# Performance work log

Measured on AMD Instinct MI355X. Metric: run time of the kernel, lower is better.

## Reference

```python
import jax, jax.numpy as jnp
import numpy as np

IN_FEATURES = 512
OUT_FEATURES = 128
KERNEL_DIM = 32
BATCH = 128


def setup_inputs() -> dict:
    key = jax.random.key(0)
    kx, kT = jax.random.split(key)
    x = jax.random.normal(kx, (BATCH, IN_FEATURES), dtype=jnp.float32)
    # nn.Parameter initialized with normal(0, 1)
    T = jax.random.normal(kT, (IN_FEATURES, OUT_FEATURES, KERNEL_DIM), dtype=jnp.float32)
    return {"x": x, "T": T}


def reference(x, T):
    B = x.shape[0]
    in_f, out_f, k_dim = T.shape
    # projection: [B, in] @ [in, out*k] -> [B, out, k]
    m = (x @ T.reshape(in_f, out_f * k_dim)).reshape(B, out_f, k_dim)
    # pairwise L1 distance over kernel dim: [B, B, out]
    # original: M = m[None], M_T = m[:, None]; norm = |M - M_T|.sum(3); o_b = exp(-norm).sum(0) - 1
    norm = jnp.abs(m[None, :, :, :] - m[:, None, :, :]).sum(axis=-1)  # [i=B, j=B, out]
    o_b = jnp.exp(-norm).sum(axis=0) - 1.0  # [B, out] (subtract self-distance term exp(0)=1)
    return jnp.concatenate([x, o_b], axis=1)  # [B, in + out]
```

## Files before the change

### kernel.cpp

```cpp
#include <hip/hip_runtime.h>

#define IN_F    512
#define NC      4096
#define OUT_COLS 640
#define B_SZ    128
#define KD      32
#define MO_PITCH 36

typedef __attribute__((ext_vector_type(8))) short  bf16x8;
typedef __attribute__((ext_vector_type(4))) float  f32x4;

static __device__ __forceinline__ unsigned short f2bfu(float f) {
    return (unsigned short)(__float_as_uint(f) >> 16);
}
static __device__ __forceinline__ unsigned int pack2(float lo, float hi) {
    return (__float_as_uint(lo) >> 16) | (__float_as_uint(hi) & 0xFFFF0000u);
}

__global__ __launch_bounds__(256) void prep_kernel(
    const float* __restrict__ x, float* __restrict__ out,
    unsigned short* __restrict__ xa)
{
    const int g = blockIdx.x * 256 + threadIdx.x;
    {
        int b = g >> 7, c4 = g & 127;
        float4 v = ((const float4*)x)[g];
        *(float4*)(out + b * OUT_COLS + c4 * 4) = v;
    }
    const int s = g >> 1, half = g & 1;
    const int mt = s >> 10, kt = (s >> 6) & 15, lane = s & 63;
    const int col = lane & 15, q = lane >> 4;
    float4 v = *(const float4*)(x + (mt * 16 + col) * IN_F + kt * 32 + q * 8 + half * 4);
    uint2 pv; pv.x = pack2(v.x, v.y); pv.y = pack2(v.z, v.w);
    *(uint2*)(xa + (size_t)s * 8 + half * 4) = pv;
}

__global__ __launch_bounds__(1024, 4) void fused_kernel(
    const unsigned short* __restrict__ xa,
    const float* __restrict__ T,
    float* __restrict__ out)
{
    __shared__ unsigned short bs[2 * 16 * 64 * 8];
    __shared__ float mo[B_SZ * MO_PITCH];
    __shared__ float psum[2 * 32 * 33];

    const int tid   = threadIdx.x;
    const int lane  = tid & 63;
    const int w     = tid >> 6;
    const int col   = lane & 15;
    const int q     = lane >> 4;
    const int o     = blockIdx.x >> 1;
    const int jhalf = blockIdx.x & 1;
    const int mt    = w >> 1, nt = w & 1;

    #pragma unroll
    for (int p = 0; p < 4; ++p) {
        int u  = tid + p * 1024;
        int kk = u >> 3, cq = u & 7;
        float4 v = *(const float4*)(T + (size_t)kk * NC + o * 32 + cq * 4);
        int kt = kk >> 5, qq = (kk >> 3) & 3, j = kk & 7;
        float e[4] = {v.x, v.y, v.z, v.w};
        #pragma unroll
        for (int r = 0; r < 4; ++r) {
            int nn = cq * 4 + r;
            int ln = qq * 16 + (nn & 15);
            bs[((((nn >> 4) * 16 + kt) * 64) + ln) * 8 + j] = f2bfu(e[r]);
        }
    }
    __syncthreads();

    f32x4 acc = {0.f, 0.f, 0.f, 0.f};
    const unsigned short* pa = xa + ((size_t)(mt * 16) * 64 + lane) * 8;
    const unsigned short* pb = bs + ((size_t)(nt * 16) * 64 + lane) * 8;
    #pragma unroll 4
    for (int kt = 0; kt < 16; ++kt) {
        bf16x8 af  = *(const bf16x8*)(pa + (size_t)kt * 512);
        bf16x8 bfr = *(const bf16x8*)(pb + (size_t)kt * 512);
        acc = __builtin_amdgcn_mfma_f32_16x16x32_bf16(af, bfr, acc, 0, 0, 0);
    }
    {
        float* dst = mo + (size_t)(mt * 16 + q * 4) * MO_PITCH + nt * 16 + col;
        dst[0 * MO_PITCH] = acc[0]; dst[1 * MO_PITCH] = acc[1];
        dst[2 * MO_PITCH] = acc[2]; dst[3 * MO_PITCH] = acc[3];
    }
    __syncthreads();

    const int jj5 = tid & 31;
    const int isl = tid >> 5;
    const int j0  = jhalf * 64 + jj5;

    float mj0[KD], mj1[KD];
    #pragma unroll
    for (int k4 = 0; k4 < 8; ++k4) {
        float4 a = *(const float4*)(mo + (size_t)j0 * MO_PITCH + k4 * 4);
        float4 b = *(const float4*)(mo + (size_t)(j0 + 32) * MO_PITCH + k4 * 4);
        mj0[k4*4+0] = a.x; mj0[k4*4+1] = a.y; mj0[k4*4+2] = a.z; mj0[k4*4+3] = a.w;
        mj1[k4*4+0] = b.x; mj1[k4*4+1] = b.y; mj1[k4*4+2] = b.z; mj1[k4*4+3] = b.w;
    }

    float s0 = 0.f, s1 = 0.f;
    #pragma unroll
    for (int ii = 0; ii < 4; ++ii) {
        const int i = isl * 4 + ii;
        float n0 = 0.f, n1 = 0.f;
        #pragma unroll
        for (int k4 = 0; k4 < 8; ++k4) {
            float4 v = *(const float4*)(mo + (size_t)i * MO_PITCH + k4 * 4);
            n0 += fabsf(mj0[k4*4+0] - v.x) + fabsf(mj0[k4*4+1] - v.y)
                + fabsf(mj0[k4*4+2] - v.z) + fabsf(mj0[k4*4+3] - v.w);
            n1 += fabsf(mj1[k4*4+0] - v.x) + fabsf(mj1[k4*4+1] - v.y)
                + fabsf(mj1[k4*4+2] - v.z) + fabsf(mj1[k4*4+3] - v.w);
        }
        s0 += __expf(-n0);
        s1 += __expf(-n1);
    }
    psum[jj5 * 33 + isl]        = s0;
    psum[1056 + jj5 * 33 + isl] = s1;
    __syncthreads();
    if (tid < 64) {
        int jsel = tid >> 5, jj = tid & 31;
        float tot = 0.f;
        #pragma unroll
        for (int u = 0; u < 32; ++u) tot += psum[jsel * 1056 + jj * 33 + u];
        out[(jhalf * 64 + jsel * 32 + jj) * OUT_COLS + IN_F + o] = tot - 1.0f;
    }
}

extern "C" void kernel_launch(void* const* d_in, const int* in_sizes, int n_in,
                              void* d_out, int out_size, void* d_ws, size_t ws_size,
                              hipStream_t stream) {
    const float* x = (const float*)d_in[0];
    const float* T = (const float*)d_in[1];
    float* out = (float*)d_out;
    unsigned short* xa = (unsigned short*)d_ws;

    prep_kernel<<<64, 256, 0, stream>>>(x, out, xa);
    fused_kernel<<<256, 1024, 0, stream>>>(xa, T, out);
}
```

Before: 71.06 us.

## Fuse prep into main kernel, halve block size, use fp16 packed L1 distances

Removes the separate prep kernel: the x copy into the output and the bf16 conversion of x now happen inside the fused kernel, with each block reading x from global memory and packing fragments in registers. Blocks shrink to 512 threads, so each wave computes two MFMA column tiles. The projection result is stored in shared memory as fp16, and the pairwise L1 distances use packed half2 subtract, abs and add instead of fp32. This saves a launch and halves the distance arithmetic, but fp16 accumulation of distances loses precision, and every block now re-reads and re-converts x.

```diff
diff --git a/kernel.cpp b/kernel.cpp
--- a/kernel.cpp
+++ b/kernel.cpp
@@ -1,14 +1,18 @@
 #include <hip/hip_runtime.h>
+#include <hip/hip_fp16.h>
 
 #define IN_F    512
 #define NC      4096
 #define OUT_COLS 640
 #define B_SZ    128
 #define KD      32
-#define MO_PITCH 36
+#define MOH_PITCH 72
 
 typedef __attribute__((ext_vector_type(8))) short  bf16x8;
 typedef __attribute__((ext_vector_type(4))) float  f32x4;
+
+union FragAB { unsigned int u[4]; bf16x8 s; };
+union H2x4   { uint4 u4; __half2 h[4]; };
 
 static __device__ __forceinline__ unsigned short f2bfu(float f) {
     return (unsigned short)(__float_as_uint(f) >> 16);
@@ -16,46 +20,38 @@
 static __device__ __forceinline__ unsigned int pack2(float lo, float hi) {
     return (__float_as_uint(lo) >> 16) | (__float_as_uint(hi) & 0xFFFF0000u);
 }
-
-__global__ __launch_bounds__(256) void prep_kernel(
-    const float* __restrict__ x, float* __restrict__ out,
-    unsigned short* __restrict__ xa)
-{
-    const int g = blockIdx.x * 256 + threadIdx.x;
-    {
-        int b = g >> 7, c4 = g & 127;
-        float4 v = ((const float4*)x)[g];
-        *(float4*)(out + b * OUT_COLS + c4 * 4) = v;
-    }
-    const int s = g >> 1, half = g & 1;
-    const int mt = s >> 10, kt = (s >> 6) & 15, lane = s & 63;
-    const int col = lane & 15, q = lane >> 4;
-    float4 v = *(const float4*)(x + (mt * 16 + col) * IN_F + kt * 32 + q * 8 + half * 4);
-    uint2 pv; pv.x = pack2(v.x, v.y); pv.y = pack2(v.z, v.w);
-    *(uint2*)(xa + (size_t)s * 8 + half * 4) = pv;
+static __device__ __forceinline__ __half2 habs2_(__half2 v) {
+    unsigned int u = *(unsigned int*)&v & 0x7FFF7FFFu;
+    return *(__half2*)&u;
 }
 
-__global__ __launch_bounds__(1024, 4) void fused_kernel(
-    const unsigned short* __restrict__ xa,
+__global__ __launch_bounds__(512, 2) void fused_kernel(
+    const float* __restrict__ x,
     const float* __restrict__ T,
     float* __restrict__ out)
 {
     __shared__ unsigned short bs[2 * 16 * 64 * 8];
-    __shared__ float mo[B_SZ * MO_PITCH];
-    __shared__ float psum[2 * 32 * 33];
+    __shared__ __half moh[B_SZ * MOH_PITCH];
+    __shared__ float psum[2 * 32 * 17];
 
     const int tid   = threadIdx.x;
     const int lane  = tid & 63;
-    const int w     = tid >> 6;
+    const int mt    = tid >> 6;
     const int col   = lane & 15;
     const int q     = lane >> 4;
     const int o     = blockIdx.x >> 1;
     const int jhalf = blockIdx.x & 1;
-    const int mt    = w >> 1, nt = w & 1;
+
+    if (tid < 64) {
+        int idx = blockIdx.x * 64 + tid;
+        int b = idx >> 7, c4 = idx & 127;
+        float4 v = ((const float4*)x)[idx];
+        *(float4*)(out + b * OUT_COLS + c4 * 4) = v;
+    }
 
     #pragma unroll
-    for (int p = 0; p < 4; ++p) {
-        int u  = tid + p * 1024;
+    for (int p = 0; p < 8; ++p) {
+        int u  = tid + p * 512;
         int kk = u >> 3, cq = u & 7;
         float4 v = *(const float4*)(T + (size_t)kk * NC + o * 32 + cq * 4);
         int kt = kk >> 5, qq = (kk >> 3) & 3, j = kk & 7;
@@ -63,65 +59,76 @@
         #pragma unroll
         for (int r = 0; r < 4; ++r) {
             int nn = cq * 4 + r;
-            int ln = qq * 16 + (nn & 15);
-            bs[((((nn >> 4) * 16 + kt) * 64) + ln) * 8 + j] = f2bfu(e[r]);
+            int slot = (((nn >> 4) * 16 + kt) * 64) + qq * 16 + (nn & 15);
+            bs[slot * 8 + j] = f2bfu(e[r]);
         }
     }
     __syncthreads();
 
-    f32x4 acc = {0.f, 0.f, 0.f, 0.f};
-    const unsigned short* pa = xa + ((size_t)(mt * 16) * 64 + lane) * 8;
-    const unsigned short* pb = bs + ((size_t)(nt * 16) * 64 + lane) * 8;
-    #pragma unroll 4
+    f32x4 acc0 = {0.f, 0.f, 0.f, 0.f}, acc1 = {0.f, 0.f, 0.f, 0.f};
+    const float* xrow = x + (size_t)(mt * 16 + col) * IN_F + q * 8;
+    #pragma unroll 8
     for (int kt = 0; kt < 16; ++kt) {
-        bf16x8 af  = *(const bf16x8*)(pa + (size_t)kt * 512);
-        bf16x8 bfr = *(const bf16x8*)(pb + (size_t)kt * 512);
-        acc = __builtin_amdgcn_mfma_f32_16x16x32_bf16(af, bfr, acc, 0, 0, 0);
+        float4 a0 = *(const float4*)(xrow + kt * 32);
+        float4 a1 = *(const float4*)(xrow + kt * 32 + 4);
+        FragAB af;
+        af.u[0] = pack2(a0.x, a0.y); af.u[1] = pack2(a0.z, a0.w);
+        af.u[2] = pack2(a1.x, a1.y); af.u[3] = pack2(a1.z, a1.w);
+        bf16x8 b0 = *(const bf16x8*)&bs[((kt      ) * 64 + lane) * 8];
+        bf16x8 b1 = *(const bf16x8*)&bs[((16 + kt) * 64 + lane) * 8];
+        acc0 = __builtin_amdgcn_mfma_f32_16x16x32_bf16(af.s, b0, acc0, 0, 0, 0);
+        acc1 = __builtin_amdgcn_mfma_f32_16x16x32_bf16(af.s, b1, acc1, 0, 0, 0);
     }
     {
-        float* dst = mo + (size_t)(mt * 16 + q * 4) * MO_PITCH + nt * 16 + col;
-        dst[0 * MO_PITCH] = acc[0]; dst[1 * MO_PITCH] = acc[1];
-        dst[2 * MO_PITCH] = acc[2]; dst[3 * MO_PITCH] = acc[3];
+        const int rowb = mt * 16 + q * 4;
+        #pragma unroll
+        for (int r = 0; r < 4; ++r) {
+            moh[(rowb + r) * MOH_PITCH + col]      = __float2half(acc0[r]);
+            moh[(rowb + r) * MOH_PITCH + 16 + col] = __float2half(acc1[r]);
+        }
     }
     __syncthreads();
 
     const int jj5 = tid & 31;
-    const int isl = tid >> 5;
+    const int isl = tid >> 4 >> 1;
     const int j0  = jhalf * 64 + jj5;
 
-    float mj0[KD], mj1[KD];
+    __half2 mj0[16], mj1[16];
     #pragma unroll
-    for (int k4 = 0; k4 < 8; ++k4) {
-        float4 a = *(const float4*)(mo + (size_t)j0 * MO_PITCH + k4 * 4);
-        float4 b = *(const float4*)(mo + (size_t)(j0 + 32) * MO_PITCH + k4 * 4);
-        mj0[k4*4+0] = a.x; mj0[k4*4+1] = a.y; mj0[k4*4+2] = a.z; mj0[k4*4+3] = a.w;
-        mj1[k4*4+0] = b.x; mj1[k4*4+1] = b.y; mj1[k4*4+2] = b.z; mj1[k4*4+3] = b.w;
+    for (int k16 = 0; k16 < 4; ++k16) {
+        H2x4 a, b;
+        a.u4 = *(const uint4*)&moh[j0 * MOH_PITCH + k16 * 8];
+        b.u4 = *(const uint4*)&moh[(j0 + 32) * MOH_PITCH + k16 * 8];
+        #pragma unroll
+        for (int h = 0; h < 4; ++h) { mj0[k16*4+h] = a.h[h]; mj1[k16*4+h] = b.h[h]; }
     }
 
     float s0 = 0.f, s1 = 0.f;
     #pragma unroll
-    for (int ii = 0; ii < 4; ++ii) {
-        const int i = isl * 4 + ii;
-        float n0 = 0.f, n1 = 0.f;
+    for (int ii = 0; ii < 8; ++ii) {
+        const int i = isl * 8 + ii;
+        __half2 n0 = __float2half2_rn(0.f), n1 = __float2half2_rn(0.f);
         #pragma unroll
-        for (int k4 = 0; k4 < 8; ++k4) {
-            float4 v = *(const float4*)(mo + (size_t)i * MO_PITCH + k4 * 4);
-            n0 += fabsf(mj0[k4*4+0] - v.x) + fabsf(mj0[k4*4+1] - v.y)
-                + fabsf(mj0[k4*4+2] - v.z) + fabsf(mj0[k4*4+3] - v.w);
-            n1 += fabsf(mj1[k4*4+0] - v.x) + fabsf(mj1[k4*4+1] - v.y)
-                + fabsf(mj1[k4*4+2] - v.z) + fabsf(mj1[k4*4+3] - v.w);
+        for (int k16 = 0; k16 < 4; ++k16) {
+            H2x4 mi; mi.u4 = *(const uint4*)&moh[i * MOH_PITCH + k16 * 8];
+            #pragma unroll
+            for (int h = 0; h < 4; ++h) {
+                n0 = __hadd2(n0, habs2_(__hsub2(mj0[k16*4+h], mi.h[h])));
+                n1 = __hadd2(n1, habs2_(__hsub2(mj1[k16*4+h], mi.h[h])));
+            }
         }
-        s0 += __expf(-n0);
-        s1 += __expf(-n1);
+        float2 f0 = __half22float2(n0), f1 = __half22float2(n1);
+        s0 += __expf(-(f0.x + f0.y));
+        s1 += __expf(-(f1.x + f1.y));
     }
-    psum[jj5 * 33 + isl]        = s0;
-    psum[1056 + jj5 * 33 + isl] = s1;
+    psum[jj5 * 17 + isl]       = s0;
+    psum[544 + jj5 * 17 + isl] = s1;
     __syncthreads();
     if (tid < 64) {
         int jsel = tid >> 5, jj = tid & 31;
         float tot = 0.f;
         #pragma unroll
-        for (int u = 0; u < 32; ++u) tot += psum[jsel * 1056 + jj * 33 + u];
+        for (int u = 0; u < 16; ++u) tot += psum[jsel * 544 + jj * 17 + u];
         out[(jhalf * 64 + jsel * 32 + jj) * OUT_COLS + IN_F + o] = tot - 1.0f;
     }
 }
@@ -132,8 +139,7 @@
     const float* x = (const float*)d_in[0];
     const float* T = (const float*)d_in[1];
     float* out = (float*)d_out;
-    unsigned short* xa = (unsigned short*)d_ws;
+    (void)d_ws; (void)ws_size;
 
-    prep_kernel<<<64, 256, 0, stream>>>(x, out, xa);
-    fused_kernel<<<256, 1024, 0, stream>>>(xa, T, out);
+    fused_kernel<<<256, 512, 0, stream>>>(x, T, out);
 }
```

After: 74.96 us. 5.5% more time.
